# Optimization experiments

Hardware: AMD Instinct MI355X
Metric: run time of the kernel (lower is better)

## Reference

```python
import jax, jax.numpy as jnp
import numpy as np

N_NODES = 100000
N_EDGES = 1600000
D = 32            # d_v = d_e = d_g = 32
LATENT = 32
IN_FEAT = 3 * D   # nodes + received-edge agg + globals
OUT_FEAT = 32


def setup_inputs() -> dict:
    key = jax.random.key(0)
    ks = jax.random.split(key, 8)
    node_attr = jax.random.normal(ks[0], (N_NODES, D), dtype=jnp.float32)
    edge_index = jax.random.randint(ks[1], (2, N_EDGES), 0, N_NODES, dtype=jnp.int64)
    edge_attr = jax.random.normal(ks[2], (N_EDGES, D), dtype=jnp.float32)
    global_attr = jax.random.normal(ks[3], (1, D), dtype=jnp.float32)
    W1 = jax.random.normal(ks[4], (IN_FEAT, LATENT), dtype=jnp.float32) * (1.0 / np.sqrt(IN_FEAT))
    b1 = jnp.zeros((LATENT,), dtype=jnp.float32)
    W2 = jax.random.normal(ks[5], (LATENT, OUT_FEAT), dtype=jnp.float32) * (1.0 / np.sqrt(LATENT))
    b2 = jnp.zeros((OUT_FEAT,), dtype=jnp.float32)
    return {"node_attr": node_attr, "edge_index": edge_index, "edge_attr": edge_attr,
            "global_attr": global_attr, "W1": W1, "b1": b1, "W2": W2, "b2": b2}


def reference(node_attr, edge_index, edge_attr, global_attr, W1, b1, W2, b2):
    receivers = edge_index[1]
    # scatter_add of edge features by receiver index -> [N, d_e]
    agg_received = jax.ops.segment_sum(edge_attr, receivers, num_segments=N_NODES)
    # broadcast global attr to all nodes -> [N, d_g]
    g = jnp.broadcast_to(global_attr, (N_NODES, global_attr.shape[1]))
    collected = jnp.concatenate([node_attr, agg_received, g], axis=-1)  # [N, 3d]
    h = jax.nn.relu(collected @ W1 + b1)
    return h @ W2 + b2
```

## Files before the change

kernel.cpp:

```cpp
#include <hip/hip_runtime.h>

#define N_NODES 100000
#define N_EDGES 1600000
#define D 32
#define NB 64
#define K_BUCKETS 1563
#define CAP 1280
#define CHUNK 8192
#define PART_BLOCKS 196
#define BINS_PAD 2048
#define CSTRIDE 16

__global__ __launch_bounds__(256) void partition_kernel(
    const int* __restrict__ receivers,
    int* __restrict__ cursor,
    unsigned int* __restrict__ slab)
{
    __shared__ int sHist[BINS_PAD];
    __shared__ int sStart[BINS_PAD];
    __shared__ int sCur[BINS_PAD];
    __shared__ int sTmp[256];
    __shared__ unsigned int sPairs[CHUNK];
    __shared__ unsigned short sBinOf[CHUNK];

    const int tid = threadIdx.x;
    const int base = blockIdx.x * CHUNK;
    const int n = min(CHUNK, N_EDGES - base);

    for (int i = tid; i < BINS_PAD; i += 256) sHist[i] = 0;
    __syncthreads();

    for (int s = 0; s < CHUNK / 256; ++s) {
        int idx = s * 256 + tid;
        if (idx < n) atomicAdd(&sHist[receivers[base + idx] >> 6], 1);
    }
    __syncthreads();

    int loc[8];
    int s = 0;
    #pragma unroll
    for (int i = 0; i < 8; ++i) {
        int v = sHist[tid * 8 + i];
        loc[i] = s;
        s += v;
    }
    sTmp[tid] = s;
    __syncthreads();
    for (int off = 1; off < 256; off <<= 1) {
        int x = sTmp[tid];
        int add = (tid >= off) ? sTmp[tid - off] : 0;
        __syncthreads();
        sTmp[tid] = x + add;
        __syncthreads();
    }
    int excl = sTmp[tid] - s;
    #pragma unroll
    for (int i = 0; i < 8; ++i) {
        int e = excl + loc[i];
        sStart[tid * 8 + i] = e;
        sCur[tid * 8 + i] = e;
    }
    __syncthreads();

    for (int s2 = 0; s2 < CHUNK / 256; ++s2) {
        int idx = s2 * 256 + tid;
        if (idx < n) {
            int r = receivers[base + idx];
            int key = r >> 6;
            int slot = atomicAdd(&sCur[key], 1);
            sPairs[slot] = ((unsigned int)(r & (NB - 1)) << 24) |
                           (unsigned int)(base + idx);
            sBinOf[slot] = (unsigned short)key;
        }
    }
    __syncthreads();

    for (int k = tid; k < K_BUCKETS; k += 256) {
        int c = sHist[k];
        int g = c ? atomicAdd(&cursor[k * CSTRIDE], c) : 0;
        sCur[k] = g - sStart[k];
    }
    __syncthreads();

    for (int idx = tid; idx < n; idx += 256) {
        int k = sBinOf[idx];
        int pos = sCur[k] + idx;
        if ((unsigned)pos < CAP) slab[(size_t)k * CAP + pos] = sPairs[idx];
    }
}

__global__ __launch_bounds__(256) void fused_kernel(
    const float* __restrict__ node_attr,
    const float* __restrict__ edge_attr,
    const unsigned int* __restrict__ slab,
    const int* __restrict__ cursor,
    const float* __restrict__ gattr,
    const float* __restrict__ W1,
    const float* __restrict__ b1,
    const float* __restrict__ W2,
    const float* __restrict__ b2,
    float* __restrict__ out)
{
    __shared__ float sW1n[1024];
    __shared__ float sW1a[1024];
    __shared__ float sW2[1024];
    __shared__ float sBase[32];
    __shared__ float sB2[32];
    __shared__ float sAgg[NB * 36];
    __shared__ float sH[NB * 36];
    __shared__ unsigned int sSorted[CAP];
    __shared__ int sCnt[NB];
    __shared__ int sStart2[NB];
    __shared__ int sCur2[NB];

    const int tid = threadIdx.x;
    for (int i = tid; i < 1024; i += 256) {
        sW1n[i] = W1[i];
        sW1a[i] = W1[1024 + i];
        sW2[i]  = W2[i];
    }
    if (tid < 32) {
        float acc = b1[tid];
        for (int k = 0; k < 32; ++k) acc += gattr[k] * W1[(64 + k) * 32 + tid];
        sBase[tid] = acc;
        sB2[tid] = b2[tid];
    }
    if (tid < NB) sCnt[tid] = 0;
    __syncthreads();

    const int b = blockIdx.x;
    const int count = min(cursor[b * CSTRIDE], CAP);
    const unsigned int* myslab = slab + (size_t)b * CAP;

    unsigned int pr[(CAP + 255) / 256];
    int np = 0;
    for (int i = tid; i < count; i += 256) {
        unsigned int p = myslab[i];
        pr[np++] = p;
        atomicAdd(&sCnt[p >> 24], 1);
    }
    __syncthreads();

    if (tid < 64) {
        int c = sCnt[tid];
        int v = c;
        #pragma unroll
        for (int off = 1; off < 64; off <<= 1) {
            int y = __shfl_up(v, off, 64);
            if (tid >= off) v += y;
        }
        sStart2[tid] = v - c;
        sCur2[tid] = v - c;
    }
    __syncthreads();

    for (int j = 0; j < np; ++j) {
        unsigned int p = pr[j];
        int slot = atomicAdd(&sCur2[p >> 24], 1);
        sSorted[slot] = p & 0xFFFFFFu;
    }
    __syncthreads();

    const int g = tid >> 2;
    const int part = tid & 3;
    const int st = sStart2[g];
    const int cn = sCnt[g];

    float a[8];
    #pragma unroll
    for (int j = 0; j < 8; ++j) a[j] = 0.0f;

    int j = 0;
    for (; j + 1 < cn; j += 2) {
        int e0 = (int)sSorted[st + j];
        int e1 = (int)sSorted[st + j + 1];
        const float* r0 = edge_attr + (size_t)e0 * D + part * 8;
        const float* r1 = edge_attr + (size_t)e1 * D + part * 8;
        float4 u0 = *(const float4*)(r0);
        float4 u1 = *(const float4*)(r0 + 4);
        float4 w0 = *(const float4*)(r1);
        float4 w1 = *(const float4*)(r1 + 4);
        a[0] += u0.x + w0.x; a[1] += u0.y + w0.y;
        a[2] += u0.z + w0.z; a[3] += u0.w + w0.w;
        a[4] += u1.x + w1.x; a[5] += u1.y + w1.y;
        a[6] += u1.z + w1.z; a[7] += u1.w + w1.w;
    }
    if (j < cn) {
        int e0 = (int)sSorted[st + j];
        const float* r0 = edge_attr + (size_t)e0 * D + part * 8;
        float4 u0 = *(const float4*)(r0);
        float4 u1 = *(const float4*)(r0 + 4);
        a[0] += u0.x; a[1] += u0.y; a[2] += u0.z; a[3] += u0.w;
        a[4] += u1.x; a[5] += u1.y; a[6] += u1.z; a[7] += u1.w;
    }
    float* dst = &sAgg[g * 36 + part * 8];
    *(float4*)(dst)     = make_float4(a[0], a[1], a[2], a[3]);
    *(float4*)(dst + 4) = make_float4(a[4], a[5], a[6], a[7]);
    __syncthreads();

    const int node = b * NB + g;
    const bool valid = (node < N_NODES);
    const int node_c = valid ? node : (N_NODES - 1);
    const int jb = part * 8;

    float h[8];
    #pragma unroll
    for (int jj = 0; jj < 8; ++jj) h[jj] = sBase[jb + jj];

    const float4* np4 = (const float4*)(node_attr + (size_t)node_c * D);
    #pragma unroll
    for (int q0 = 0; q0 < 8; ++q0) {
        float4 xv = np4[q0];
        float xk[4] = {xv.x, xv.y, xv.z, xv.w};
        #pragma unroll
        for (int kk = 0; kk < 4; ++kk) {
            int k = 4 * q0 + kk;
            float4 w0 = *(const float4*)&sW1n[k * 32 + jb];
            float4 w1 = *(const float4*)&sW1n[k * 32 + jb + 4];
            h[0] += xk[kk] * w0.x; h[1] += xk[kk] * w0.y;
            h[2] += xk[kk] * w0.z; h[3] += xk[kk] * w0.w;
            h[4] += xk[kk] * w1.x; h[5] += xk[kk] * w1.y;
            h[6] += xk[kk] * w1.z; h[7] += xk[kk] * w1.w;
        }
    }
    #pragma unroll 8
    for (int k = 0; k < 32; ++k) {
        float ak = sAgg[g * 36 + k];
        float4 w0 = *(const float4*)&sW1a[k * 32 + jb];
        float4 w1 = *(const float4*)&sW1a[k * 32 + jb + 4];
        h[0] += ak * w0.x; h[1] += ak * w0.y;
        h[2] += ak * w0.z; h[3] += ak * w0.w;
        h[4] += ak * w1.x; h[5] += ak * w1.y;
        h[6] += ak * w1.z; h[7] += ak * w1.w;
    }
    {
        float* hd = &sH[g * 36 + jb];
        #pragma unroll
        for (int jj = 0; jj < 8; ++jj) hd[jj] = fmaxf(h[jj], 0.0f);
    }
    __syncthreads();

    float o[8];
    #pragma unroll
    for (int jj = 0; jj < 8; ++jj) o[jj] = sB2[jb + jj];
    #pragma unroll 8
    for (int k = 0; k < 32; ++k) {
        float hk = sH[g * 36 + k];
        float4 w0 = *(const float4*)&sW2[k * 32 + jb];
        float4 w1 = *(const float4*)&sW2[k * 32 + jb + 4];
        o[0] += hk * w0.x; o[1] += hk * w0.y;
        o[2] += hk * w0.z; o[3] += hk * w0.w;
        o[4] += hk * w1.x; o[5] += hk * w1.y;
        o[6] += hk * w1.z; o[7] += hk * w1.w;
    }

    if (valid) {
        float4* op4 = (float4*)(out + (size_t)node * D + jb);
        op4[0] = make_float4(o[0], o[1], o[2], o[3]);
        op4[1] = make_float4(o[4], o[5], o[6], o[7]);
    }
}

extern "C" void kernel_launch(void* const* d_in, const int* in_sizes, int n_in,
                              void* d_out, int out_size, void* d_ws, size_t ws_size,
                              hipStream_t stream) {
    const float* node_attr  = (const float*)d_in[0];
    const int*   edge_index = (const int*)d_in[1];
    const float* edge_attr  = (const float*)d_in[2];
    const float* gattr      = (const float*)d_in[3];
    const float* W1         = (const float*)d_in[4];
    const float* b1         = (const float*)d_in[5];
    const float* W2         = (const float*)d_in[6];
    const float* b2         = (const float*)d_in[7];
    float* out = (float*)d_out;

    const int* receivers = edge_index + N_EDGES;

    int* cursor = (int*)d_ws;
    unsigned int* slab =
        (unsigned int*)d_ws + (size_t)BINS_PAD * CSTRIDE;

    hipMemsetAsync(cursor, 0, (size_t)BINS_PAD * CSTRIDE * sizeof(int), stream);

    partition_kernel<<<PART_BLOCKS, 256, 0, stream>>>(receivers, cursor, slab);

    fused_kernel<<<K_BUCKETS, 256, 0, stream>>>(
        node_attr, edge_attr, slab, cursor,
        gattr, W1, b1, W2, b2, out);
}
```

Before: 366.6 us.

## Halve partition chunk, cache receivers in registers, unroll gather, reuse shared buffer

The partition kernel now handles 4096-edge chunks across twice as many blocks, and keeps each thread's receiver values in registers so they are not loaded from global memory a second time. The fused kernel drops the per-thread pair array and re-reads the slab instead, cutting register use. The edge gather is unrolled to four edges per iteration for more memory-level parallelism. The hidden activations now reuse the aggregation shared buffer behind an extra barrier, freeing shared memory that may allow more resident blocks.

Measured after the change: 367.9 us. About the same (+0.3%).

```diff
diff --git a/kernel.cpp b/kernel.cpp
--- a/kernel.cpp
+++ b/kernel.cpp
@@ -6,8 +6,8 @@
 #define NB 64
 #define K_BUCKETS 1563
 #define CAP 1280
-#define CHUNK 8192
-#define PART_BLOCKS 196
+#define CHUNK 4096
+#define PART_BLOCKS ((N_EDGES + CHUNK - 1) / CHUNK)
 #define BINS_PAD 2048
 #define CSTRIDE 16
 
@@ -30,9 +30,12 @@
     for (int i = tid; i < BINS_PAD; i += 256) sHist[i] = 0;
     __syncthreads();
 
-    for (int s = 0; s < CHUNK / 256; ++s) {
-        int idx = s * 256 + tid;
-        if (idx < n) atomicAdd(&sHist[receivers[base + idx] >> 6], 1);
+    int rr[16];
+    #pragma unroll
+    for (int i = 0; i < 16; ++i) {
+        int idx = i * 256 + tid;
+        rr[i] = (idx < n) ? receivers[base + idx] : -1;
+        if (rr[i] >= 0) atomicAdd(&sHist[rr[i] >> 6], 1);
     }
     __syncthreads();
 
@@ -62,13 +65,13 @@
     }
     __syncthreads();
 
-    for (int s2 = 0; s2 < CHUNK / 256; ++s2) {
-        int idx = s2 * 256 + tid;
-        if (idx < n) {
-            int r = receivers[base + idx];
-            int key = r >> 6;
+    #pragma unroll
+    for (int i = 0; i < 16; ++i) {
+        if (rr[i] >= 0) {
+            int idx = i * 256 + tid;
+            int key = rr[i] >> 6;
             int slot = atomicAdd(&sCur[key], 1);
-            sPairs[slot] = ((unsigned int)(r & (NB - 1)) << 24) |
+            sPairs[slot] = ((unsigned int)(rr[i] & (NB - 1)) << 24) |
                            (unsigned int)(base + idx);
             sBinOf[slot] = (unsigned short)key;
         }
@@ -107,7 +110,6 @@
     __shared__ float sBase[32];
     __shared__ float sB2[32];
     __shared__ float sAgg[NB * 36];
-    __shared__ float sH[NB * 36];
     __shared__ unsigned int sSorted[CAP];
     __shared__ int sCnt[NB];
     __shared__ int sStart2[NB];
@@ -132,13 +134,8 @@
     const int count = min(cursor[b * CSTRIDE], CAP);
     const unsigned int* myslab = slab + (size_t)b * CAP;
 
-    unsigned int pr[(CAP + 255) / 256];
-    int np = 0;
-    for (int i = tid; i < count; i += 256) {
-        unsigned int p = myslab[i];
-        pr[np++] = p;
-        atomicAdd(&sCnt[p >> 24], 1);
-    }
+    for (int i = tid; i < count; i += 256)
+        atomicAdd(&sCnt[myslab[i] >> 24], 1);
     __syncthreads();
 
     if (tid < 64) {
@@ -154,8 +151,8 @@
     }
     __syncthreads();
 
-    for (int j = 0; j < np; ++j) {
-        unsigned int p = pr[j];
+    for (int i = tid; i < count; i += 256) {
+        unsigned int p = myslab[i];
         int slot = atomicAdd(&sCur2[p >> 24], 1);
         sSorted[slot] = p & 0xFFFFFFu;
     }
@@ -165,43 +162,58 @@
     const int part = tid & 3;
     const int st = sStart2[g];
     const int cn = sCnt[g];
+    const int fo = part * 8;
 
     float a[8];
     #pragma unroll
     for (int j = 0; j < 8; ++j) a[j] = 0.0f;
 
     int j = 0;
-    for (; j + 1 < cn; j += 2) {
+    for (; j + 3 < cn; j += 4) {
         int e0 = (int)sSorted[st + j];
         int e1 = (int)sSorted[st + j + 1];
-        const float* r0 = edge_attr + (size_t)e0 * D + part * 8;
-        const float* r1 = edge_attr + (size_t)e1 * D + part * 8;
+        int e2 = (int)sSorted[st + j + 2];
+        int e3 = (int)sSorted[st + j + 3];
+        const float* r0 = edge_attr + (size_t)e0 * D + fo;
+        const float* r1 = edge_attr + (size_t)e1 * D + fo;
+        const float* r2 = edge_attr + (size_t)e2 * D + fo;
+        const float* r3 = edge_attr + (size_t)e3 * D + fo;
         float4 u0 = *(const float4*)(r0);
         float4 u1 = *(const float4*)(r0 + 4);
-        float4 w0 = *(const float4*)(r1);
-        float4 w1 = *(const float4*)(r1 + 4);
-        a[0] += u0.x + w0.x; a[1] += u0.y + w0.y;
-        a[2] += u0.z + w0.z; a[3] += u0.w + w0.w;
-        a[4] += u1.x + w1.x; a[5] += u1.y + w1.y;
-        a[6] += u1.z + w1.z; a[7] += u1.w + w1.w;
-    }
-    if (j < cn) {
+        float4 v0 = *(const float4*)(r1);
+        float4 v1 = *(const float4*)(r1 + 4);
+        float4 w0 = *(const float4*)(r2);
+        float4 w1 = *(const float4*)(r2 + 4);
+        float4 x0 = *(const float4*)(r3);
+        float4 x1 = *(const float4*)(r3 + 4);
+        a[0] += (u0.x + v0.x) + (w0.x + x0.x);
+        a[1] += (u0.y + v0.y) + (w0.y + x0.y);
+        a[2] += (u0.z + v0.z) + (w0.z + x0.z);
+        a[3] += (u0.w + v0.w) + (w0.w + x0.w);
+        a[4] += (u1.x + v1.x) + (w1.x + x1.x);
+        a[5] += (u1.y + v1.y) + (w1.y + x1.y);
+        a[6] += (u1.z + v1.z) + (w1.z + x1.z);
+        a[7] += (u1.w + v1.w) + (w1.w + x1.w);
+    }
+    for (; j < cn; ++j) {
         int e0 = (int)sSorted[st + j];
-        const float* r0 = edge_attr + (size_t)e0 * D + part * 8;
+        const float* r0 = edge_attr + (size_t)e0 * D + fo;
         float4 u0 = *(const float4*)(r0);
         float4 u1 = *(const float4*)(r0 + 4);
         a[0] += u0.x; a[1] += u0.y; a[2] += u0.z; a[3] += u0.w;
         a[4] += u1.x; a[5] += u1.y; a[6] += u1.z; a[7] += u1.w;
     }
-    float* dst = &sAgg[g * 36 + part * 8];
-    *(float4*)(dst)     = make_float4(a[0], a[1], a[2], a[3]);
-    *(float4*)(dst + 4) = make_float4(a[4], a[5], a[6], a[7]);
+    {
+        float* dst = &sAgg[g * 36 + fo];
+        *(float4*)(dst)     = make_float4(a[0], a[1], a[2], a[3]);
+        *(float4*)(dst + 4) = make_float4(a[4], a[5], a[6], a[7]);
+    }
     __syncthreads();
 
     const int node = b * NB + g;
     const bool valid = (node < N_NODES);
     const int node_c = valid ? node : (N_NODES - 1);
-    const int jb = part * 8;
+    const int jb = fo;
 
     float h[8];
     #pragma unroll
@@ -233,8 +245,9 @@
         h[4] += ak * w1.x; h[5] += ak * w1.y;
         h[6] += ak * w1.z; h[7] += ak * w1.w;
     }
+    __syncthreads();
     {
-        float* hd = &sH[g * 36 + jb];
+        float* hd = &sAgg[g * 36 + jb];
         #pragma unroll
         for (int jj = 0; jj < 8; ++jj) hd[jj] = fmaxf(h[jj], 0.0f);
     }
@@ -245,7 +258,7 @@
     for (int jj = 0; jj < 8; ++jj) o[jj] = sB2[jb + jj];
     #pragma unroll 8
     for (int k = 0; k < 32; ++k) {
-        float hk = sH[g * 36 + k];
+        float hk = sAgg[g * 36 + k];
         float4 w0 = *(const float4*)&sW2[k * 32 + jb];
         float4 w1 = *(const float4*)&sW2[k * 32 + jb + 4];
         o[0] += hk * w0.x; o[1] += hk * w0.y;
```
